# Performance work log

Measured on AMD Instinct MI355X. Metric: run time of the kernel, lower is better.

Reference implementation:

```python
import jax, jax.numpy as jnp
import numpy as np

IMG = 224      # img_size
P = 16         # patch_size
C = 3          # in_chans
K = 100        # n_segments
COMPACT = 10.0 # slic compactness
ITERS = 10     # slic k-means iterations


def _resize_matrix(src, dst):
    # Linear antialiased resize is a linear map; materialize it by resizing identity.
    return jax.image.resize(jnp.eye(src, dtype=jnp.float32), (dst, src),
                            method='linear', antialias=True)


def _slic_labels(img_hwc):
    """Simplified SLIC: grid-initialized k-means in (color, compactness-scaled xy) space."""
    H, W = IMG, IMG
    S = float(np.sqrt(H * W / K))         # superpixel spacing
    ratio = COMPACT / S                   # spatial scaling (SLIC distance weighting)
    yy, xx = jnp.meshgrid(jnp.arange(H, dtype=jnp.float32),
                          jnp.arange(W, dtype=jnp.float32), indexing='ij')
    feat = jnp.concatenate([img_hwc, (yy * ratio)[..., None], (xx * ratio)[..., None]],
                           axis=-1).reshape(H * W, C + 2)  # [HW, 5]
    # grid init of K centers
    gh = int(np.ceil(np.sqrt(K)))
    gw = int(np.ceil(K / gh))
    cy = ((np.arange(gh) + 0.5) * H / gh).astype(np.int32)
    cx = ((np.arange(gw) + 0.5) * W / gw).astype(np.int32)
    idx = (cy[:, None] * W + cx[None, :]).reshape(-1)[:K]
    centers0 = feat[jnp.asarray(idx)]  # [K, 5]

    f2 = jnp.sum(feat * feat, axis=1, keepdims=True)  # [HW,1]

    def dists(centers):
        c2 = jnp.sum(centers * centers, axis=1)  # [K]
        return f2 + c2[None, :] - 2.0 * (feat @ centers.T)  # [HW,K]

    def body(i, centers):
        lbl = jnp.argmin(dists(centers), axis=1)              # [HW]
        oh = jax.nn.one_hot(lbl, K, dtype=feat.dtype)         # [HW,K]
        cnt = oh.sum(0)                                       # [K]
        new = (oh.T @ feat) / jnp.maximum(cnt, 1.0)[:, None]  # [K,5]
        return jnp.where((cnt > 0)[:, None], new, centers)

    centers = jax.lax.fori_loop(0, ITERS, body, centers0)
    return jnp.argmin(dists(centers), axis=1).reshape(H, W)


def _embed_one(img_chw, A):
    img = jnp.transpose(img_chw, (1, 2, 0))                     # [H,W,C]
    labels = jax.lax.stop_gradient(_slic_labels(img))           # [H,W] int
    masks = jax.nn.one_hot(labels, K, dtype=img.dtype, axis=0)  # [K,H,W]
    masked = masks[..., None] * img[None]                       # [K,H,W,C]
    tmp = jnp.einsum('ph,khwc->kpwc', A, masked)                # resize rows
    return jnp.einsum('qw,kpwc->kpqc', A, tmp)                  # [K,P,P,C]


def reference(x):
    B = x.shape[0]
    A = _resize_matrix(IMG, P)
    sp = jax.vmap(lambda im: _embed_one(im, A))(x)  # [B,K,P,P,C]
    # torch: view(B, K*C, P, P)  (raw row-major reinterpret), flatten(2), transpose(1,2)
    out = sp.reshape(B, K * C, P, P).reshape(B, K * C, P * P)
    return jnp.transpose(out, (0, 2, 1))  # [B, P*P, K*C]


def setup_inputs() -> dict:
    key = jax.random.key(0)
    x = jax.random.uniform(key, (8, C, IMG, IMG), dtype=jnp.float32)
    return {"x": x}
```

## Files before the change

### kernel.cpp

```cpp
#include <hip/hip_runtime.h>
#include <math.h>

#define IMGD 224
#define HW 50176
#define NK 100
#define NB 8
#define OUT_PER_B 76800
#define NCHUNK 131
#define MSTR 13


static __device__ __forceinline__ float ratio_f32() {
  return (float)(10.0 / sqrt(224.0 * 224.0 / 100.0));
}

static __device__ __forceinline__ float dist5s(float f0, float f1, float f2,
                                               float f3, float f4, float fsq,
                                               float c0, float c1, float c2,
                                               float c3, float c4, float q) {
  float dot = __fmul_rn(f0, c0);
  dot = __fmaf_rn(f1, c1, dot);
  dot = __fmaf_rn(f2, c2, dot);
  dot = __fmaf_rn(f3, c3, dot);
  dot = __fmaf_rn(f4, c4, dot);
  return __fsub_rn(__fadd_rn(fsq, q), __fmul_rn(2.0f, dot));
}

static __device__ __forceinline__ float fsq5(float f0, float f1, float f2,
                                             float f3, float f4) {
  float s = __fmul_rn(f0, f0);
  s = __fadd_rn(s, __fmul_rn(f1, f1));
  s = __fadd_rn(s, __fmul_rn(f2, f2));
  s = __fadd_rn(s, __fmul_rn(f3, f3));
  s = __fadd_rn(s, __fmul_rn(f4, f4));
  return s;
}

__global__ void __launch_bounds__(256, 2) iter_kernel(
    const float* __restrict__ x, float* __restrict__ centers,
    const float* __restrict__ c2g, float* __restrict__ partials, int flag,
    float* __restrict__ Ag) {
  __shared__ float4 ck4[NK];
  __shared__ float2 ck2[NK];
  __shared__ unsigned int maskS[2][NK * MSTR];
  __shared__ unsigned short ppkS[2][NK * MSTR];
  __shared__ float4 cval4[2][384];
  __shared__ float  cvalf[2][384];
  __shared__ int cntS[2][128];
  __shared__ int offxS[2][128];
  __shared__ int wtotS[2];
  __shared__ float ubpart[2][12][10];
  __shared__ float ubg[2][12];
  __shared__ unsigned int candm[2][12][4];
  __shared__ unsigned char clist[2][12][104];
  __shared__ int clen[2][12];
  __shared__ float ared[128];
  int bx = blockIdx.x, b = blockIdx.y;
  int tid = threadIdx.x;

  if (bx >= 66) {
    for (int rr = 0; rr < 2; ++rr) {
      int p = 2 * b + rr;
      float cp = (p + 0.5f) * 14.0f - 0.5f;
      if (tid < 128) {
        float xd0 = fabsf(cp - (float)tid) / 14.0f;
        float trip0 = fmaxf(0.0f, 1.0f - xd0);
        float trip1 = 0.0f;
        int t2 = tid + 128;
        if (t2 < IMGD) {
          float xd = fabsf(cp - (float)t2) / 14.0f;
          trip1 = fmaxf(0.0f, 1.0f - xd);
        }
        ared[tid] = trip0 + trip1;
      }
      __syncthreads();
      for (int s = 64; s > 0; s >>= 1) {
        if (tid < s) ared[tid] += ared[tid + s];
        __syncthreads();
      }
      float Zp = ared[0];
      __syncthreads();
      if (tid < IMGD) {
        float xd = fabsf(cp - (float)tid) / 14.0f;
        Ag[p * IMGD + tid] = fmaxf(0.0f, 1.0f - xd) / Zp;
      }
      __syncthreads();
    }
    return;
  }

  int half = tid >> 7;
  int lt = tid & 127;
  int c = 2 * bx + half;
  int start, len;
  if (c < NCHUNK) {
    start = (c < 129) ? c * 384 : 49536 + (c - 129) * 320;
    len   = (c < 129) ? 384 : 320;
  } else {
    start = 0; len = 0;
  }

  const float ratio = ratio_f32();
  const float* x0 = x + (size_t)b * 3 * HW;
  if (flag == 0) {
    if (tid < NK) {
      int gy = tid / 10, gx = tid - 10 * (tid / 10);
      int cy = (int)((gy + 0.5) * 224.0 / 10.0);
      int cx = (int)((gx + 0.5) * 224.0 / 10.0);
      int i = cy * IMGD + cx;
      float c0 = x0[i], c1 = x0[HW + i], c2 = x0[2 * HW + i];
      float c3 = __fmul_rn((float)cy, ratio);
      float c4 = __fmul_rn((float)cx, ratio);
      float s = __fmul_rn(c0, c0);
      s = __fadd_rn(s, __fmul_rn(c1, c1));
      s = __fadd_rn(s, __fmul_rn(c2, c2));
      s = __fadd_rn(s, __fmul_rn(c3, c3));
      s = __fadd_rn(s, __fmul_rn(c4, c4));
      ck4[tid] = make_float4(c0, c1, c2, c3);
      ck2[tid] = make_float2(c4, s);
      if (bx == 0) {
        float* oc = centers + ((size_t)b * NK + tid) * 5;
        oc[0] = c0; oc[1] = c1; oc[2] = c2; oc[3] = c3; oc[4] = c4;
      }
    }
  } else {
    const float* cb = centers + (size_t)b * NK * 5;
    const float* c2b = c2g + (size_t)b * NK;
    if (tid < NK) {
      ck4[tid] = make_float4(cb[tid*5+0], cb[tid*5+1], cb[tid*5+2], cb[tid*5+3]);
      ck2[tid] = make_float2(cb[tid*5+4], c2b[tid]);
    }
  }
  for (int t = lt; t < NK * MSTR; t += 128) maskS[half][t] = 0u;
  if (lt < 48) candm[half][lt >> 2][lt & 3] = 0u;

  float f0[3], f1[3], f2[3], f3[3], f4[3], fq[3];
  bool vld[3];
  for (int r = 0; r < 3; ++r) {
    int t = lt + r * 128;
    vld[r] = (t < len);
    int i = start + (vld[r] ? t : 0);
    int y = i / IMGD, xw = i - y * IMGD;
    f0[r] = x0[i]; f1[r] = x0[HW + i]; f2[r] = x0[2 * HW + i];
    f3[r] = __fmul_rn((float)y, ratio);
    f4[r] = __fmul_rn((float)xw, ratio);
    fq[r] = fsq5(f0[r], f1[r], f2[r], f3[r], f4[r]);
  }
  __syncthreads();

  if (lt < 120) {
    int g = lt / 10, kb = lt - 10 * g;
    int i0 = start + g * 32, i1 = i0 + 31;
    int ymin = i0 / IMGD, ymax = i1 / IMGD;
    int cmin = (ymin == ymax) ? (i0 - ymin * IMGD) : 0;
    int cmax = (ymin == ymax) ? (i1 - ymax * IMGD) : (IMGD - 1);
    float f3mn = __fmul_rn((float)ymin, ratio);
    float f3mx = __fmul_rn((float)ymax, ratio);
    float f4mn = __fmul_rn((float)cmin, ratio);
    float f4mx = __fmul_rn((float)cmax, ratio);
    float mn = 3.4e38f;
    for (int k = kb * 10; k < kb * 10 + 10; ++k) {
      float c3 = ck4[k].w, c4 = ck2[k].x;
      float dy = fmaxf(fabsf(c3 - f3mn), fabsf(c3 - f3mx));
      float dx = fmaxf(fabsf(c4 - f4mn), fabsf(c4 - f4mx));
      mn = fminf(mn, dy * dy + dx * dx + 3.0f);
    }
    ubpart[half][g][kb] = mn;
  }
  __syncthreads();
  if (lt < 12) {
    float mn = ubpart[half][lt][0];
    for (int j = 1; j < 10; ++j) mn = fminf(mn, ubpart[half][lt][j]);
    ubg[half][lt] = mn + 1.0f;
  }
  __syncthreads();
  if (lt < 120) {
    int g = lt / 10, kb = lt - 10 * g;
    int i0 = start + g * 32, i1 = i0 + 31;
    int ymin = i0 / IMGD, ymax = i1 / IMGD;
    int cmin = (ymin == ymax) ? (i0 - ymin * IMGD) : 0;
    int cmax = (ymin == ymax) ? (i1 - ymax * IMGD) : (IMGD - 1);
    float f3mn = __fmul_rn((float)ymin, ratio);
    float f3mx = __fmul_rn((float)ymax, ratio);
    float f4mn = __fmul_rn((float)cmin, ratio);
    float f4mx = __fmul_rn((float)cmax, ratio);
    float lim = ubg[half][g];
    for (int k = kb * 10; k < kb * 10 + 10; ++k) {
      float c3 = ck4[k].w, c4 = ck2[k].x;
      float dy = fmaxf(0.0f, fmaxf(f3mn - c3, c3 - f3mx));
      float dx = fmaxf(0.0f, fmaxf(f4mn - c4, c4 - f4mx));
      if (dy * dy + dx * dx <= lim)
        atomicOr(&candm[half][g][k >> 5], 1u << (k & 31));
    }
  }
  __syncthreads();
  if (lt < 12) {
    int len2 = 0;
    for (int w = 0; w < 4; ++w) {
      unsigned int m = candm[half][lt][w];
      while (m) {
        int j = __ffs(m) - 1;
        m &= m - 1;
        clist[half][lt][len2++] = (unsigned char)(w * 32 + j);
      }
    }
    clen[half][lt] = len2;
  }
  __syncthreads();

  float best[3]; int bk[3];
  for (int r = 0; r < 3; ++r) {
    best[r] = 3.4e38f; bk[r] = 0;
    int t = lt + r * 128;
    int g = (t < 384) ? (t >> 5) : 0;
    int n = clen[half][g];
    for (int j = 0; j < n; ++j) {
      int k = clist[half][g][j];
      float4 a4 = ck4[k];
      float2 a2 = ck2[k];
      float d = dist5s(f0[r], f1[r], f2[r], f3[r], f4[r], fq[r],
                       a4.x, a4.y, a4.z, a4.w, a2.x, a2.y);
      if (d < best[r]) { best[r] = d; bk[r] = k; }
    }
  }
  for (int r = 0; r < 3; ++r) {
    int t = lt + r * 128;
    if (vld[r]) atomicOr(&maskS[half][bk[r] * MSTR + (t >> 5)], 1u << (t & 31));
  }
  __syncthreads();

  int myCnt = 0;
  if (lt < NK) {
    int s = 0;
    for (int g = 0; g < 12; ++g) {
      ppkS[half][lt * MSTR + g] = (unsigned short)s;
      s += __popc(maskS[half][lt * MSTR + g]);
    }
    myCnt = s;
  }
  cntS[half][lt] = myCnt;
  __syncthreads();

  int v = myCnt;
  for (int d = 1; d < 64; d <<= 1) {
    int u = __shfl_up(v, d, 64);
    if ((tid & 63) >= d) v += u;
  }
  if (lt == 63) wtotS[half] = v;
  __syncthreads();
  if (lt >= 64) v += wtotS[half];
  offxS[half][lt] = v;
  __syncthreads();

  for (int r = 0; r < 3; ++r) {
    int t = lt + r * 128;
    if (vld[r]) {
      int g = t >> 5, j = t & 31;
      unsigned int m = maskS[half][bk[r] * MSTR + g];
      int rank = ppkS[half][bk[r] * MSTR + g] + __popc(m & ((1u << j) - 1u));
      int pos = offxS[half][bk[r]] - cntS[half][bk[r]] + rank;
      cval4[half][pos] = make_float4(f0[r], f1[r], f2[r], f3[r]);
      cvalf[half][pos] = f4[r];
    }
  }
  __syncthreads();

  if (c < NCHUNK && lt < NK) {
    int n = cntS[half][lt];
    int base = offxS[half][lt] - n;
    float s0 = 0.f, s1 = 0.f, s2 = 0.f, s3 = 0.f, s4 = 0.f, s5 = 0.f;
    for (int m = 0; m < n; ++m) {
      float4 vv = cval4[half][base + m];
      float ww = cvalf[half][base + m];
      s0 = __fadd_rn(s0, vv.x);
      s1 = __fadd_rn(s1, vv.y);
      s2 = __fadd_rn(s2, vv.z);
      s3 = __fadd_rn(s3, vv.w);
      s4 = __fadd_rn(s4, ww);
      s5 += 1.0f;
    }
    float* pp = partials + ((size_t)(b * NK + lt) * 6) * NCHUNK + c;
    pp[0 * NCHUNK] = s0; pp[1 * NCHUNK] = s1; pp[2 * NCHUNK] = s2;
    pp[3 * NCHUNK] = s3; pp[4 * NCHUNK] = s4; pp[5 * NCHUNK] = s5;
  }
}

__global__ void __launch_bounds__(128) combine_update_kernel(
    float* __restrict__ centers, const float* __restrict__ partials,
    float* __restrict__ c2g) {
  __shared__ float st[8 * 6 * NCHUNK];
  __shared__ float sums[8][6];
  __shared__ float newc[8][5];
  int bb = blockIdx.x;
  int tid = threadIdx.x;
  const float* base = partials + (size_t)bb * 8 * 6 * NCHUNK;
  for (int t = tid; t < 8 * 6 * NCHUNK; t += 128) st[t] = base[t];
  __syncthreads();
  if (tid < 48) {
    int row = tid / 6, comp = tid - 6 * (tid / 6);
    const float* rp = st + (row * 6 + comp) * NCHUNK;
    float s = rp[0];
    for (int c = 1; c < NCHUNK; ++c) s = __fadd_rn(s, rp[c]);
    sums[row][comp] = s;
  }
  __syncthreads();
  if (tid < 40) {
    int row = tid / 5, d = tid - 5 * (tid / 5);
    float cntv = sums[row][5];
    float* cc = centers + (size_t)(bb * 8 + row) * 5;
    float v;
    if (cntv > 0.0f) {
      float m = fmaxf(cntv, 1.0f);
      v = __fdiv_rn(sums[row][d], m);
      cc[d] = v;
    } else {
      v = cc[d];
    }
    newc[row][d] = v;
  }
  __syncthreads();
  if (tid < 8) {
    float t0 = __fmul_rn(newc[tid][0], newc[tid][0]);
    t0 = __fadd_rn(t0, __fmul_rn(newc[tid][1], newc[tid][1]));
    t0 = __fadd_rn(t0, __fmul_rn(newc[tid][2], newc[tid][2]));
    t0 = __fadd_rn(t0, __fmul_rn(newc[tid][3], newc[tid][3]));
    t0 = __fadd_rn(t0, __fmul_rn(newc[tid][4], newc[tid][4]));
    c2g[bb * 8 + tid] = t0;
  }
}

__global__ void __launch_bounds__(128, 4) label_kernel(
    const float* __restrict__ x, const float* __restrict__ centers,
    const float* __restrict__ c2g, unsigned char* __restrict__ labels) {
  __shared__ float4 ck4[NK];
  __shared__ float2 ck2[NK];
  __shared__ float ubpart[12][10];
  __shared__ float ubg[12];
  __shared__ unsigned int candm[12][4];
  int c = blockIdx.x, b = blockIdx.y;
  int tid = threadIdx.x;
  int start = (c < 129) ? c * 384 : 49536 + (c - 129) * 320;
  int len   = (c < 129) ? 384 : 320;

  const float ratio = ratio_f32();
  const float* x0 = x + (size_t)b * 3 * HW;
  const float* cb = centers + (size_t)b * NK * 5;
  const float* c2b = c2g + (size_t)b * NK;
  if (tid < NK) {
    ck4[tid] = make_float4(cb[tid*5+0], cb[tid*5+1], cb[tid*5+2], cb[tid*5+3]);
    ck2[tid] = make_float2(cb[tid*5+4], c2b[tid]);
  }
  if (tid < 48) candm[tid >> 2][tid & 3] = 0u;

  float f0[3], f1[3], f2[3], f3[3], f4[3], fq[3];
  int ii[3];
  bool vld[3];
  for (int r = 0; r < 3; ++r) {
    int t = tid + r * 128;
    vld[r] = (t < len);
    int i = start + (vld[r] ? t : 0);
    ii[r] = i;
    int y = i / IMGD, xw = i - y * IMGD;
    f0[r] = x0[i]; f1[r] = x0[HW + i]; f2[r] = x0[2 * HW + i];
    f3[r] = __fmul_rn((float)y, ratio);
    f4[r] = __fmul_rn((float)xw, ratio);
    fq[r] = fsq5(f0[r], f1[r], f2[r], f3[r], f4[r]);
  }
  __syncthreads();

  if (tid < 120) {
    int g = tid / 10, kb = tid - 10 * g;
    int i0 = start + g * 32, i1 = i0 + 31;
    int ymin = i0 / IMGD, ymax = i1 / IMGD;
    int cmin = (ymin == ymax) ? (i0 - ymin * IMGD) : 0;
    int cmax = (ymin == ymax) ? (i1 - ymax * IMGD) : (IMGD - 1);
    float f3mn = __fmul_rn((float)ymin, ratio);
    float f3mx = __fmul_rn((float)ymax, ratio);
    float f4mn = __fmul_rn((float)cmin, ratio);
    float f4mx = __fmul_rn((float)cmax, ratio);
    float mn = 3.4e38f;
    for (int k = kb * 10; k < kb * 10 + 10; ++k) {
      float c3 = ck4[k].w, c4 = ck2[k].x;
      float dy = fmaxf(fabsf(c3 - f3mn), fabsf(c3 - f3mx));
      float dx = fmaxf(fabsf(c4 - f4mn), fabsf(c4 - f4mx));
      mn = fminf(mn, dy * dy + dx * dx + 3.0f);
    }
    ubpart[g][kb] = mn;
  }
  __syncthreads();
  if (tid < 12) {
    float mn = ubpart[tid][0];
    for (int j = 1; j < 10; ++j) mn = fminf(mn, ubpart[tid][j]);
    ubg[tid] = mn + 1.0f;
  }
  __syncthreads();
  if (tid < 120) {
    int g = tid / 10, kb = tid - 10 * g;
    int i0 = start + g * 32, i1 = i0 + 31;
    int ymin = i0 / IMGD, ymax = i1 / IMGD;
    int cmin = (ymin == ymax) ? (i0 - ymin * IMGD) : 0;
    int cmax = (ymin == ymax) ? (i1 - ymax * IMGD) : (IMGD - 1);
    float f3mn = __fmul_rn((float)ymin, ratio);
    float f3mx = __fmul_rn((float)ymax, ratio);
    float f4mn = __fmul_rn((float)cmin, ratio);
    float f4mx = __fmul_rn((float)cmax, ratio);
    float lim = ubg[g];
    for (int k = kb * 10; k < kb * 10 + 10; ++k) {
      float c3 = ck4[k].w, c4 = ck2[k].x;
      float dy = fmaxf(0.0f, fmaxf(f3mn - c3, c3 - f3mx));
      float dx = fmaxf(0.0f, fmaxf(f4mn - c4, c4 - f4mx));
      if (dy * dy + dx * dx <= lim)
        atomicOr(&candm[g][k >> 5], 1u << (k & 31));
    }
  }
  __syncthreads();

  float best[3]; int bk[3];
  for (int r = 0; r < 3; ++r) {
    best[r] = 3.4e38f; bk[r] = 0;
    int t = tid + r * 128;
    int g = (t < 384) ? (t >> 5) : 0;
    for (int w = 0; w < 4; ++w) {
      unsigned int m = candm[g][w];
      while (m) {
        int j = __ffs(m) - 1;
        m &= m - 1;
        int k = (w << 5) + j;
        float4 a4 = ck4[k];
        float2 a2 = ck2[k];
        float d = dist5s(f0[r], f1[r], f2[r], f3[r], f4[r], fq[r],
                         a4.x, a4.y, a4.z, a4.w, a2.x, a2.y);
        if (d < best[r]) { best[r] = d; bk[r] = k; }
      }
    }
  }
  unsigned char* lb = labels + (size_t)b * HW;
  for (int r = 0; r < 3; ++r)
    if (vld[r]) lb[ii[r]] = (unsigned char)bk[r];
}

__global__ void __launch_bounds__(256) embed_kernel(
    const float* __restrict__ x, const unsigned char* __restrict__ labels,
    const float* __restrict__ Ag, float* __restrict__ out) {
  __shared__ float Apv[28];
  __shared__ float Aqw[4][28];
  __shared__ float sk[4][NK * 3];
  int b = blockIdx.y;
  int p = blockIdx.x >> 2;
  int qg = blockIdx.x & 3;
  int q0 = qg * 4;
  int tid = threadIdx.x;

  int h0 = max(0, 14 * p - 7), h1 = min(IMGD - 1, 14 * p + 20);
  int hl = h1 - h0 + 1;
  int w0q[4], w1q[4];
#pragma unroll
  for (int qi = 0; qi < 4; ++qi) {
    int q = q0 + qi;
    w0q[qi] = max(0, 14 * q - 7);
    w1q[qi] = min(IMGD - 1, 14 * q + 20);
  }
  int W0 = w0q[0], W1 = w1q[3];
  int WU = W1 - W0 + 1;

  if (tid < hl) Apv[tid] = Ag[p * IMGD + h0 + tid];
  {
    int t = tid - 64;
    if (t >= 0 && t < 112) {
      int qi = t / 28, dw = t - 28 * qi;
      if (dw <= w1q[qi] - w0q[qi])
        Aqw[qi][dw] = Ag[(q0 + qi) * IMGD + w0q[qi] + dw];
    }
  }
  for (int t = tid; t < 4 * NK * 3; t += 256) sk[t / (NK * 3)][t % (NK * 3)] = 0.0f;
  __syncthreads();

  const float* xb = x + (size_t)b * 3 * HW;
  const unsigned char* lb = labels + (size_t)b * HW;
  int n = hl * WU;
  for (int r = 0; r < 8; ++r) {
    int idx = tid + r * 256;
    if (idx >= n) break;
    int dh = idx / WU;
    int dcol = idx - dh * WU;
    int col = W0 + dcol;
    int i = (h0 + dh) * IMGD + col;
    float v0 = xb[i], v1 = xb[HW + i], v2 = xb[2 * HW + i];
    int k = lb[i];
    float ap = Apv[dh];
#pragma unroll
    for (int qi = 0; qi < 4; ++qi) {
      if (col >= w0q[qi] && col <= w1q[qi]) {
        float wgt = ap * Aqw[qi][col - w0q[qi]];
        atomicAdd(&sk[qi][k * 3 + 0], wgt * v0);
        atomicAdd(&sk[qi][k * 3 + 1], wgt * v1);
        atomicAdd(&sk[qi][k * 3 + 2], wgt * v2);
      }
    }
  }
  __syncthreads();

  float* outb = out + (size_t)b * OUT_PER_B;
  for (int t = tid; t < 4 * NK * 3; t += 256) {
    int qi = t / (NK * 3), t3 = t - qi * (NK * 3);
    int k = t3 / 3, cc = t3 - 3 * k;
    int base = p * 48 + (q0 + qi) * 3;
    int f = k * 768 + base + cc;
    outb[(f & 255) * 300 + (f >> 8)] = sk[qi][t3];
  }
}

extern "C" void kernel_launch(void* const* d_in, const int* in_sizes, int n_in,
                              void* d_out, int out_size, void* d_ws, size_t ws_size,
                              hipStream_t stream) {
  const float* x = (const float*)d_in[0];
  float* out = (float*)d_out;
  char* ws = (char*)d_ws;
  float* centers        = (float*)(ws + 16384);
  float* c2g            = (float*)(ws + 49152);
  float* Ag             = (float*)(ws + 65536);
  unsigned char* labels = (unsigned char*)(ws + 98304);
  float* partials       = (float*)(ws + 1703936);

  dim3 ig0(67, NB);
  dim3 ig(66, NB);
  iter_kernel<<<ig0, 256, 0, stream>>>(x, centers, c2g, partials, 0, Ag);
  combine_update_kernel<<<NB * NK / 8, 128, 0, stream>>>(centers, partials, c2g);
  for (int it = 1; it < 10; ++it) {
    iter_kernel<<<ig, 256, 0, stream>>>(x, centers, c2g, partials, 1, Ag);
    combine_update_kernel<<<NB * NK / 8, 128, 0, stream>>>(centers, partials, c2g);
  }
  label_kernel<<<dim3(NCHUNK, NB), 128, 0, stream>>>(x, centers, c2g, labels);
  dim3 egrid(64, NB);
  embed_kernel<<<egrid, 256, 0, stream>>>(x, labels, Ag, out);
}
```

Before: 296.0 us.

## Fuse final labeling into embed kernel and inline candidate iteration in iter kernel

Removes the separate label kernel and its label buffer. The embed kernel now computes each pixel's nearest center itself, using a per-block candidate set pruned by a spatial bound over the block's row and column window. The iter kernel drops the compacted candidate list and its extra barrier, walking the candidate bitmask directly. The combine kernel now uses 256 threads and float4 loads to stage partials. Trade-off: pixels in overlapping resize windows get their labels recomputed by several embed blocks, and the wider per-block window may admit more candidate centers.

```diff
diff --git a/kernel.cpp b/kernel.cpp
--- a/kernel.cpp
+++ b/kernel.cpp
@@ -52,8 +52,6 @@
   __shared__ float ubpart[2][12][10];
   __shared__ float ubg[2][12];
   __shared__ unsigned int candm[2][12][4];
-  __shared__ unsigned char clist[2][12][104];
-  __shared__ int clen[2][12];
   __shared__ float ared[128];
   int bx = blockIdx.x, b = blockIdx.y;
   int tid = threadIdx.x;
@@ -194,33 +192,24 @@
     }
   }
   __syncthreads();
-  if (lt < 12) {
-    int len2 = 0;
-    for (int w = 0; w < 4; ++w) {
-      unsigned int m = candm[half][lt][w];
-      while (m) {
-        int j = __ffs(m) - 1;
-        m &= m - 1;
-        clist[half][lt][len2++] = (unsigned char)(w * 32 + j);
-      }
-    }
-    clen[half][lt] = len2;
-  }
-  __syncthreads();
 
   float best[3]; int bk[3];
   for (int r = 0; r < 3; ++r) {
     best[r] = 3.4e38f; bk[r] = 0;
     int t = lt + r * 128;
     int g = (t < 384) ? (t >> 5) : 0;
-    int n = clen[half][g];
-    for (int j = 0; j < n; ++j) {
-      int k = clist[half][g][j];
-      float4 a4 = ck4[k];
-      float2 a2 = ck2[k];
-      float d = dist5s(f0[r], f1[r], f2[r], f3[r], f4[r], fq[r],
-                       a4.x, a4.y, a4.z, a4.w, a2.x, a2.y);
-      if (d < best[r]) { best[r] = d; bk[r] = k; }
+    for (int w = 0; w < 4; ++w) {
+      unsigned int m = candm[half][g][w];
+      while (m) {
+        int j = __ffs(m) - 1;
+        m &= m - 1;
+        int k = (w << 5) + j;
+        float4 a4 = ck4[k];
+        float2 a2 = ck2[k];
+        float d = dist5s(f0[r], f1[r], f2[r], f3[r], f4[r], fq[r],
+                         a4.x, a4.y, a4.z, a4.w, a2.x, a2.y);
+        if (d < best[r]) { best[r] = d; bk[r] = k; }
+      }
     }
   }
   for (int r = 0; r < 3; ++r) {
@@ -285,7 +274,7 @@
   }
 }
 
-__global__ void __launch_bounds__(128) combine_update_kernel(
+__global__ void __launch_bounds__(256) combine_update_kernel(
     float* __restrict__ centers, const float* __restrict__ partials,
     float* __restrict__ c2g) {
   __shared__ float st[8 * 6 * NCHUNK];
@@ -294,7 +283,8 @@
   int bb = blockIdx.x;
   int tid = threadIdx.x;
   const float* base = partials + (size_t)bb * 8 * 6 * NCHUNK;
-  for (int t = tid; t < 8 * 6 * NCHUNK; t += 128) st[t] = base[t];
+  for (int t = tid; t < (8 * 6 * NCHUNK) / 4; t += 256)
+    ((float4*)st)[t] = ((const float4*)base)[t];
   __syncthreads();
   if (tid < 48) {
     int row = tid / 6, comp = tid - 6 * (tid / 6);
@@ -329,122 +319,17 @@
   }
 }
 
-__global__ void __launch_bounds__(128, 4) label_kernel(
+__global__ void __launch_bounds__(256) embed_kernel(
     const float* __restrict__ x, const float* __restrict__ centers,
-    const float* __restrict__ c2g, unsigned char* __restrict__ labels) {
-  __shared__ float4 ck4[NK];
-  __shared__ float2 ck2[NK];
-  __shared__ float ubpart[12][10];
-  __shared__ float ubg[12];
-  __shared__ unsigned int candm[12][4];
-  int c = blockIdx.x, b = blockIdx.y;
-  int tid = threadIdx.x;
-  int start = (c < 129) ? c * 384 : 49536 + (c - 129) * 320;
-  int len   = (c < 129) ? 384 : 320;
-
-  const float ratio = ratio_f32();
-  const float* x0 = x + (size_t)b * 3 * HW;
-  const float* cb = centers + (size_t)b * NK * 5;
-  const float* c2b = c2g + (size_t)b * NK;
-  if (tid < NK) {
-    ck4[tid] = make_float4(cb[tid*5+0], cb[tid*5+1], cb[tid*5+2], cb[tid*5+3]);
-    ck2[tid] = make_float2(cb[tid*5+4], c2b[tid]);
-  }
-  if (tid < 48) candm[tid >> 2][tid & 3] = 0u;
-
-  float f0[3], f1[3], f2[3], f3[3], f4[3], fq[3];
-  int ii[3];
-  bool vld[3];
-  for (int r = 0; r < 3; ++r) {
-    int t = tid + r * 128;
-    vld[r] = (t < len);
-    int i = start + (vld[r] ? t : 0);
-    ii[r] = i;
-    int y = i / IMGD, xw = i - y * IMGD;
-    f0[r] = x0[i]; f1[r] = x0[HW + i]; f2[r] = x0[2 * HW + i];
-    f3[r] = __fmul_rn((float)y, ratio);
-    f4[r] = __fmul_rn((float)xw, ratio);
-    fq[r] = fsq5(f0[r], f1[r], f2[r], f3[r], f4[r]);
-  }
-  __syncthreads();
-
-  if (tid < 120) {
-    int g = tid / 10, kb = tid - 10 * g;
-    int i0 = start + g * 32, i1 = i0 + 31;
-    int ymin = i0 / IMGD, ymax = i1 / IMGD;
-    int cmin = (ymin == ymax) ? (i0 - ymin * IMGD) : 0;
-    int cmax = (ymin == ymax) ? (i1 - ymax * IMGD) : (IMGD - 1);
-    float f3mn = __fmul_rn((float)ymin, ratio);
-    float f3mx = __fmul_rn((float)ymax, ratio);
-    float f4mn = __fmul_rn((float)cmin, ratio);
-    float f4mx = __fmul_rn((float)cmax, ratio);
-    float mn = 3.4e38f;
-    for (int k = kb * 10; k < kb * 10 + 10; ++k) {
-      float c3 = ck4[k].w, c4 = ck2[k].x;
-      float dy = fmaxf(fabsf(c3 - f3mn), fabsf(c3 - f3mx));
-      float dx = fmaxf(fabsf(c4 - f4mn), fabsf(c4 - f4mx));
-      mn = fminf(mn, dy * dy + dx * dx + 3.0f);
-    }
-    ubpart[g][kb] = mn;
-  }
-  __syncthreads();
-  if (tid < 12) {
-    float mn = ubpart[tid][0];
-    for (int j = 1; j < 10; ++j) mn = fminf(mn, ubpart[tid][j]);
-    ubg[tid] = mn + 1.0f;
-  }
-  __syncthreads();
-  if (tid < 120) {
-    int g = tid / 10, kb = tid - 10 * g;
-    int i0 = start + g * 32, i1 = i0 + 31;
-    int ymin = i0 / IMGD, ymax = i1 / IMGD;
-    int cmin = (ymin == ymax) ? (i0 - ymin * IMGD) : 0;
-    int cmax = (ymin == ymax) ? (i1 - ymax * IMGD) : (IMGD - 1);
-    float f3mn = __fmul_rn((float)ymin, ratio);
-    float f3mx = __fmul_rn((float)ymax, ratio);
-    float f4mn = __fmul_rn((float)cmin, ratio);
-    float f4mx = __fmul_rn((float)cmax, ratio);
-    float lim = ubg[g];
-    for (int k = kb * 10; k < kb * 10 + 10; ++k) {
-      float c3 = ck4[k].w, c4 = ck2[k].x;
-      float dy = fmaxf(0.0f, fmaxf(f3mn - c3, c3 - f3mx));
-      float dx = fmaxf(0.0f, fmaxf(f4mn - c4, c4 - f4mx));
-      if (dy * dy + dx * dx <= lim)
-        atomicOr(&candm[g][k >> 5], 1u << (k & 31));
-    }
-  }
-  __syncthreads();
-
-  float best[3]; int bk[3];
-  for (int r = 0; r < 3; ++r) {
-    best[r] = 3.4e38f; bk[r] = 0;
-    int t = tid + r * 128;
-    int g = (t < 384) ? (t >> 5) : 0;
-    for (int w = 0; w < 4; ++w) {
-      unsigned int m = candm[g][w];
-      while (m) {
-        int j = __ffs(m) - 1;
-        m &= m - 1;
-        int k = (w << 5) + j;
-        float4 a4 = ck4[k];
-        float2 a2 = ck2[k];
-        float d = dist5s(f0[r], f1[r], f2[r], f3[r], f4[r], fq[r],
-                         a4.x, a4.y, a4.z, a4.w, a2.x, a2.y);
-        if (d < best[r]) { best[r] = d; bk[r] = k; }
-      }
-    }
-  }
-  unsigned char* lb = labels + (size_t)b * HW;
-  for (int r = 0; r < 3; ++r)
-    if (vld[r]) lb[ii[r]] = (unsigned char)bk[r];
-}
-
-__global__ void __launch_bounds__(256) embed_kernel(
-    const float* __restrict__ x, const unsigned char* __restrict__ labels,
-    const float* __restrict__ Ag, float* __restrict__ out) {
+    const float* __restrict__ c2g, const float* __restrict__ Ag,
+    float* __restrict__ out) {
   __shared__ float Apv[28];
   __shared__ float Aqw[4][28];
   __shared__ float sk[4][NK * 3];
+  __shared__ float4 ck4[NK];
+  __shared__ float2 ck2[NK];
+  __shared__ float ubk[128];
+  __shared__ unsigned int candm[4];
   int b = blockIdx.y;
   int p = blockIdx.x >> 2;
   int qg = blockIdx.x & 3;
@@ -463,6 +348,12 @@
   int W0 = w0q[0], W1 = w1q[3];
   int WU = W1 - W0 + 1;
 
+  const float* cb = centers + (size_t)b * NK * 5;
+  const float* c2b = c2g + (size_t)b * NK;
+  if (tid < NK) {
+    ck4[tid] = make_float4(cb[tid*5+0], cb[tid*5+1], cb[tid*5+2], cb[tid*5+3]);
+    ck2[tid] = make_float2(cb[tid*5+4], c2b[tid]);
+  }
   if (tid < hl) Apv[tid] = Ag[p * IMGD + h0 + tid];
   {
     int t = tid - 64;
@@ -472,11 +363,42 @@
         Aqw[qi][dw] = Ag[(q0 + qi) * IMGD + w0q[qi] + dw];
     }
   }
-  for (int t = tid; t < 4 * NK * 3; t += 256) sk[t / (NK * 3)][t % (NK * 3)] = 0.0f;
+  for (int t = tid; t < 4 * NK * 3; t += 256)
+    sk[t / (NK * 3)][t % (NK * 3)] = 0.0f;
+  if (tid < 4) candm[tid] = 0u;
+  __syncthreads();
+
+  const float ratio = ratio_f32();
+  float f3mn = __fmul_rn((float)h0, ratio);
+  float f3mx = __fmul_rn((float)h1, ratio);
+  float f4mn = __fmul_rn((float)W0, ratio);
+  float f4mx = __fmul_rn((float)W1, ratio);
+  if (tid < 128) {
+    float u = 3.4e38f;
+    if (tid < NK) {
+      float c3 = ck4[tid].w, c4 = ck2[tid].x;
+      float dy = fmaxf(fabsf(c3 - f3mn), fabsf(c3 - f3mx));
+      float dx = fmaxf(fabsf(c4 - f4mn), fabsf(c4 - f4mx));
+      u = dy * dy + dx * dx + 3.0f;
+    }
+    ubk[tid] = u;
+  }
+  __syncthreads();
+  for (int s = 64; s > 0; s >>= 1) {
+    if (tid < s) ubk[tid] = fminf(ubk[tid], ubk[tid + s]);
+    __syncthreads();
+  }
+  float lim = ubk[0] + 1.0f;
+  if (tid < NK) {
+    float c3 = ck4[tid].w, c4 = ck2[tid].x;
+    float dy = fmaxf(0.0f, fmaxf(f3mn - c3, c3 - f3mx));
+    float dx = fmaxf(0.0f, fmaxf(f4mn - c4, c4 - f4mx));
+    if (dy * dy + dx * dx <= lim)
+      atomicOr(&candm[tid >> 5], 1u << (tid & 31));
+  }
   __syncthreads();
 
   const float* xb = x + (size_t)b * 3 * HW;
-  const unsigned char* lb = labels + (size_t)b * HW;
   int n = hl * WU;
   for (int r = 0; r < 8; ++r) {
     int idx = tid + r * 256;
@@ -484,17 +406,34 @@
     int dh = idx / WU;
     int dcol = idx - dh * WU;
     int col = W0 + dcol;
-    int i = (h0 + dh) * IMGD + col;
+    int hh = h0 + dh;
+    int i = hh * IMGD + col;
     float v0 = xb[i], v1 = xb[HW + i], v2 = xb[2 * HW + i];
-    int k = lb[i];
+    float f3 = __fmul_rn((float)hh, ratio);
+    float f4 = __fmul_rn((float)col, ratio);
+    float fq = fsq5(v0, v1, v2, f3, f4);
+    float bestd = 3.4e38f; int bk = 0;
+    for (int w = 0; w < 4; ++w) {
+      unsigned int m = candm[w];
+      while (m) {
+        int j = __ffs(m) - 1;
+        m &= m - 1;
+        int k = (w << 5) + j;
+        float4 a4 = ck4[k];
+        float2 a2 = ck2[k];
+        float d = dist5s(v0, v1, v2, f3, f4, fq,
+                         a4.x, a4.y, a4.z, a4.w, a2.x, a2.y);
+        if (d < bestd) { bestd = d; bk = k; }
+      }
+    }
     float ap = Apv[dh];
 #pragma unroll
     for (int qi = 0; qi < 4; ++qi) {
       if (col >= w0q[qi] && col <= w1q[qi]) {
         float wgt = ap * Aqw[qi][col - w0q[qi]];
-        atomicAdd(&sk[qi][k * 3 + 0], wgt * v0);
-        atomicAdd(&sk[qi][k * 3 + 1], wgt * v1);
-        atomicAdd(&sk[qi][k * 3 + 2], wgt * v2);
+        atomicAdd(&sk[qi][bk * 3 + 0], wgt * v0);
+        atomicAdd(&sk[qi][bk * 3 + 1], wgt * v1);
+        atomicAdd(&sk[qi][bk * 3 + 2], wgt * v2);
       }
     }
   }
@@ -516,21 +455,19 @@
   const float* x = (const float*)d_in[0];
   float* out = (float*)d_out;
   char* ws = (char*)d_ws;
-  float* centers        = (float*)(ws + 16384);
-  float* c2g            = (float*)(ws + 49152);
-  float* Ag             = (float*)(ws + 65536);
-  unsigned char* labels = (unsigned char*)(ws + 98304);
-  float* partials       = (float*)(ws + 1703936);
+  float* centers  = (float*)(ws + 16384);
+  float* c2g      = (float*)(ws + 49152);
+  float* Ag       = (float*)(ws + 65536);
+  float* partials = (float*)(ws + 1703936);
 
   dim3 ig0(67, NB);
   dim3 ig(66, NB);
   iter_kernel<<<ig0, 256, 0, stream>>>(x, centers, c2g, partials, 0, Ag);
-  combine_update_kernel<<<NB * NK / 8, 128, 0, stream>>>(centers, partials, c2g);
+  combine_update_kernel<<<NB * NK / 8, 256, 0, stream>>>(centers, partials, c2g);
   for (int it = 1; it < 10; ++it) {
     iter_kernel<<<ig, 256, 0, stream>>>(x, centers, c2g, partials, 1, Ag);
-    combine_update_kernel<<<NB * NK / 8, 128, 0, stream>>>(centers, partials, c2g);
-  }
-  label_kernel<<<dim3(NCHUNK, NB), 128, 0, stream>>>(x, centers, c2g, labels);
+    combine_update_kernel<<<NB * NK / 8, 256, 0, stream>>>(centers, partials, c2g);
+  }
   dim3 egrid(64, NB);
-  embed_kernel<<<egrid, 256, 0, stream>>>(x, labels, Ag, out);
-}
+  embed_kernel<<<egrid, 256, 0, stream>>>(x, centers, c2g, Ag, out);
+}
```

Result: slower. 308.9 us (+4.3%).
